# Kernel optimization log

Hardware: AMD Instinct MI355X
Metric: run time of the kernel (lower is better)

## Reference

```python
import jax, jax.numpy as jnp
import numpy as np

B, S, F, O = 128, 8, 32, 16  # batch, board_size, in_features, out_features
D = 2 * S - 1                # diff_size = 15 relative offsets per axis


def setup_inputs() -> dict:
    key = jax.random.key(0)
    k1, k2, k3 = jax.random.split(key, 3)
    inp = jax.random.normal(k1, (B, S, S, F), dtype=jnp.float32)
    # torch.nn.Bilinear init: U(-1/sqrt(in1_features), 1/sqrt(in1_features))
    bound = 1.0 / np.sqrt(F)
    W = jax.random.uniform(k2, (D, D, O, F, F), jnp.float32, -bound, bound)
    b = jax.random.uniform(k3, (D, D, O), jnp.float32, -bound, bound)
    return {"inp": inp, "W": W, "b": b}


def reference(inp, W, b):
    # inp: (B, S, S, F); W: (D, D, O, F, F); b: (D, D, O)
    s = inp.shape[1]
    idx = jnp.arange(s)
    # offset index: off[a, bb] = bb - a + (s - 1), in [0, 2s-2]
    off = idx[None, :] - idx[:, None] + (s - 1)  # (S, S)
    # gather per-pair bilinear weights: Wg[ax, bx, ay, by] = W[bx-ax+7, by-ay+7]
    Wg = W[off[:, :, None, None], off[None, None, :, :]]  # (S,S,S,S,O,F,F)
    bg = b[off[:, :, None, None], off[None, None, :, :]]  # (S,S,S,S,O) [ax,bx,ay,by]
    # out[b, ax, ay, bx, by, o] = a_i W_oij b_j + bias_o
    out = jnp.einsum('bxyi,xXyYoij,bXYj->bxyXYo', inp, Wg, inp)
    out = out + bg.transpose(0, 2, 1, 3, 4)[None]  # bias to [ax,ay,bx,by,o]
    return out
```

## Files before the change

kernel.cpp:

```cpp
#include <hip/hip_runtime.h>

typedef _Float16 f16;
typedef _Float16 f16x8 __attribute__((ext_vector_type(8)));
typedef float f32x4 __attribute__((ext_vector_type(4)));
typedef unsigned int u32;
typedef const __attribute__((address_space(1))) u32* gas1_t;
typedef __attribute__((address_space(3))) u32* las3_t;

#define WGRAN 460800
#define IGRAN 32768

__global__ __launch_bounds__(256) void convert_kernel(
    const float* __restrict__ W, const float* __restrict__ inp,
    f16* __restrict__ W_h, f16* __restrict__ inp_h)
{
    const int g = blockIdx.x * 256 + threadIdx.x;
    if (g < WGRAN) {
        const int dxdy = g >> 11;
        const int r = g & 2047;
        const int i = r >> 6, o = (r >> 2) & 15, quad = r & 3;
        const float* src = W + (size_t)dxdy * 16384 + o * 1024 + i * 32 + quad * 8;
        const float4 v0 = *(const float4*)src;
        const float4 v1 = *(const float4*)(src + 4);
        f16x8 h = { (f16)v0.x, (f16)v0.y, (f16)v0.z, (f16)v0.w,
                    (f16)v1.x, (f16)v1.y, (f16)v1.z, (f16)v1.w };
        *(f16x8*)(W_h + (size_t)g * 8) = h;
    } else {
        const int k = g - WGRAN;
        const float* src = inp + (size_t)k * 8;
        const float4 v0 = *(const float4*)src;
        const float4 v1 = *(const float4*)(src + 4);
        f16x8 h = { (f16)v0.x, (f16)v0.y, (f16)v0.z, (f16)v0.w,
                    (f16)v1.x, (f16)v1.y, (f16)v1.z, (f16)v1.w };
        *(f16x8*)(inp_h + (size_t)k * 8) = h;
    }
}

__global__ __launch_bounds__(256, 5) void rel_mfma3(
    const f16* __restrict__ W_h,
    const f16* __restrict__ inp_h,
    const float* __restrict__ bias,
    float* __restrict__ out)
{
    extern __shared__ __align__(16) f16 Wl[];

    const int hw = blockIdx.x;
    const int bid = ((hw & 7) << 9) | (hw >> 3);
    const int Y = bid & 7, X = (bid >> 3) & 7, y = (bid >> 6) & 7, x = (bid >> 9) & 7;
    const int dx = X - x + 7, dy = Y - y + 7;
    const int dxdy = dx * 15 + dy;

    const int t = threadIdx.x;

    {
        const f16* base = W_h + (size_t)dxdy * 16384;
        #pragma unroll
        for (int it = 0; it < 8; ++it) {
            const int idx = (it * 256 + t) * 8;
            __builtin_amdgcn_global_load_lds((gas1_t)(base + idx),
                                             (las3_t)&Wl[idx], 16, 0, 0);
        }
    }

    const int lane = t & 63;
    const int wave = t >> 6;
    const int quad = lane >> 4;
    const int m = lane & 15;

    f16x8 a0[4], a1[4], c0, c1;
    {
        const int b0 = wave * 32 + m;
        const int b1 = b0 + 16;
        const f16* ar0 = inp_h + ((b0 * 8 + x) * 8 + y) * 32;
        const f16* ar1 = inp_h + ((b1 * 8 + x) * 8 + y) * 32;
        #pragma unroll
        for (int g = 0; g < 4; ++g) {
            a0[g] = *(const f16x8*)(ar0 + g * 8);
            a1[g] = *(const f16x8*)(ar1 + g * 8);
        }
        c0 = *(const f16x8*)(inp_h + ((b0 * 8 + X) * 8 + Y) * 32 + quad * 8);
        c1 = *(const f16x8*)(inp_h + ((b1 * 8 + X) * 8 + Y) * 32 + quad * 8);
    }

    __syncthreads();

    f32x4 acc0 = {0.f, 0.f, 0.f, 0.f};
    f32x4 acc1 = {0.f, 0.f, 0.f, 0.f};
    const f16* wl = &Wl[m * 32 + quad * 8];
    f16x8 bfrag = *(const f16x8*)(wl);
    #pragma unroll
    for (int kb = 0; kb < 32; ++kb) {
        const f16x8 bcur = bfrag;
        if (kb < 31)
            bfrag = *(const f16x8*)(wl + (kb + 1) * 512);
        const f16 av0 = a0[kb >> 3][kb & 7];
        const f16 av1 = a1[kb >> 3][kb & 7];
        const f16x8 af0 = c0 * av0;
        const f16x8 af1 = c1 * av1;
        acc0 = __builtin_amdgcn_mfma_f32_16x16x32_f16(af0, bcur, acc0, 0, 0, 0);
        acc1 = __builtin_amdgcn_mfma_f32_16x16x32_f16(af1, bcur, acc1, 0, 0, 0);
    }

    const float bv = bias[dxdy * 16 + m];
    #pragma unroll
    for (int r = 0; r < 4; ++r) {
        const int b0 = wave * 32 + quad * 4 + r;
        out[((size_t)b0 * 4096 + bid) * 16 + m] = acc0[r] + bv;
        out[((size_t)(b0 + 16) * 4096 + bid) * 16 + m] = acc1[r] + bv;
    }
}

extern "C" void kernel_launch(void* const* d_in, const int* in_sizes, int n_in,
                              void* d_out, int out_size, void* d_ws, size_t ws_size,
                              hipStream_t stream)
{
    const float* inp  = (const float*)d_in[0];
    const float* W    = (const float*)d_in[1];
    const float* bias = (const float*)d_in[2];
    float* out = (float*)d_out;

    f16* W_h   = (f16*)d_ws;
    f16* inp_h = (f16*)d_ws + (size_t)WGRAN * 8;

    hipLaunchKernelGGL(convert_kernel, dim3((WGRAN + IGRAN) / 256), dim3(256), 0,
                       stream, W, inp, W_h, inp_h);
    hipLaunchKernelGGL(rel_mfma3, dim3(4096), dim3(256), 32768, stream,
                       W_h, inp_h, bias, out);
}
```

Before: 105.6 us.

## Loop over Y per block with double-buffered LDS weight prefetch

Each block now handles all 8 Y positions for a fixed (x,y,X), loading input rows once and iterating Y. The next Y's weight slice is prefetched into a second LDS buffer while the current one is consumed. This cuts the block count eightfold and doubles LDS use, reducing parallelism and occupancy in exchange for overlap and reuse.

```diff
diff --git a/kernel.cpp b/kernel.cpp
--- a/kernel.cpp
+++ b/kernel.cpp
@@ -36,7 +36,7 @@
     }
 }
 
-__global__ __launch_bounds__(256, 5) void rel_mfma3(
+__global__ __launch_bounds__(256, 2) void rel_mfma4(
     const f16* __restrict__ W_h,
     const f16* __restrict__ inp_h,
     const float* __restrict__ bias,
@@ -45,32 +45,28 @@
     extern __shared__ __align__(16) f16 Wl[];
 
     const int hw = blockIdx.x;
-    const int bid = ((hw & 7) << 9) | (hw >> 3);
-    const int Y = bid & 7, X = (bid >> 3) & 7, y = (bid >> 6) & 7, x = (bid >> 9) & 7;
-    const int dx = X - x + 7, dy = Y - y + 7;
-    const int dxdy = dx * 15 + dy;
+    const int X = hw & 7, y = (hw >> 3) & 7, x = (hw >> 6) & 7;
+    const int dx = X - x + 7;
 
     const int t = threadIdx.x;
-
-    {
-        const f16* base = W_h + (size_t)dxdy * 16384;
-        #pragma unroll
-        for (int it = 0; it < 8; ++it) {
-            const int idx = (it * 256 + t) * 8;
-            __builtin_amdgcn_global_load_lds((gas1_t)(base + idx),
-                                             (las3_t)&Wl[idx], 16, 0, 0);
-        }
-    }
-
     const int lane = t & 63;
     const int wave = t >> 6;
     const int quad = lane >> 4;
     const int m = lane & 15;
 
-    f16x8 a0[4], a1[4], c0, c1;
+    const f16* wbase = W_h + (size_t)(dx * 15 + 7 - y) * 16384;
+
+    #pragma unroll
+    for (int it = 0; it < 8; ++it) {
+        const int idx = (it * 256 + t) * 8;
+        __builtin_amdgcn_global_load_lds((gas1_t)(wbase + idx),
+                                         (las3_t)&Wl[idx], 16, 0, 0);
+    }
+
+    f16x8 a0[4], a1[4], c0[8], c1[8];
+    const int b0 = wave * 32 + m;
+    const int b1 = b0 + 16;
     {
-        const int b0 = wave * 32 + m;
-        const int b1 = b0 + 16;
         const f16* ar0 = inp_h + ((b0 * 8 + x) * 8 + y) * 32;
         const f16* ar1 = inp_h + ((b1 * 8 + x) * 8 + y) * 32;
         #pragma unroll
@@ -78,35 +74,62 @@
             a0[g] = *(const f16x8*)(ar0 + g * 8);
             a1[g] = *(const f16x8*)(ar1 + g * 8);
         }
-        c0 = *(const f16x8*)(inp_h + ((b0 * 8 + X) * 8 + Y) * 32 + quad * 8);
-        c1 = *(const f16x8*)(inp_h + ((b1 * 8 + X) * 8 + Y) * 32 + quad * 8);
+        const f16* cr0 = inp_h + (b0 * 8 + X) * 256 + quad * 8;
+        const f16* cr1 = inp_h + (b1 * 8 + X) * 256 + quad * 8;
+        #pragma unroll
+        for (int Yi = 0; Yi < 8; ++Yi) {
+            c0[Yi] = *(const f16x8*)(cr0 + Yi * 32);
+            c1[Yi] = *(const f16x8*)(cr1 + Yi * 32);
+        }
     }
 
     __syncthreads();
 
-    f32x4 acc0 = {0.f, 0.f, 0.f, 0.f};
-    f32x4 acc1 = {0.f, 0.f, 0.f, 0.f};
-    const f16* wl = &Wl[m * 32 + quad * 8];
-    f16x8 bfrag = *(const f16x8*)(wl);
+    const int bid_base = ((x * 8 + y) * 8 + X) * 8;
+
     #pragma unroll
-    for (int kb = 0; kb < 32; ++kb) {
-        const f16x8 bcur = bfrag;
-        if (kb < 31)
-            bfrag = *(const f16x8*)(wl + (kb + 1) * 512);
-        const f16 av0 = a0[kb >> 3][kb & 7];
-        const f16 av1 = a1[kb >> 3][kb & 7];
-        const f16x8 af0 = c0 * av0;
-        const f16x8 af1 = c1 * av1;
-        acc0 = __builtin_amdgcn_mfma_f32_16x16x32_f16(af0, bcur, acc0, 0, 0, 0);
-        acc1 = __builtin_amdgcn_mfma_f32_16x16x32_f16(af1, bcur, acc1, 0, 0, 0);
-    }
+    for (int Y = 0; Y < 8; ++Y) {
+        const int cur = Y & 1;
 
-    const float bv = bias[dxdy * 16 + m];
-    #pragma unroll
-    for (int r = 0; r < 4; ++r) {
-        const int b0 = wave * 32 + quad * 4 + r;
-        out[((size_t)b0 * 4096 + bid) * 16 + m] = acc0[r] + bv;
-        out[((size_t)(b0 + 16) * 4096 + bid) * 16 + m] = acc1[r] + bv;
+        if (Y < 7) {
+            const f16* nbase = wbase + (size_t)(Y + 1) * 16384;
+            f16* ldst = Wl + (cur ^ 1) * 16384;
+            #pragma unroll
+            for (int it = 0; it < 8; ++it) {
+                const int idx = (it * 256 + t) * 8;
+                __builtin_amdgcn_global_load_lds((gas1_t)(nbase + idx),
+                                                 (las3_t)&ldst[idx], 16, 0, 0);
+            }
+        }
+
+        f32x4 acc0 = {0.f, 0.f, 0.f, 0.f};
+        f32x4 acc1 = {0.f, 0.f, 0.f, 0.f};
+        const f16* wl = Wl + cur * 16384 + m * 32 + quad * 8;
+        f16x8 bfrag = *(const f16x8*)(wl);
+        #pragma unroll
+        for (int kb = 0; kb < 32; ++kb) {
+            const f16x8 bcur = bfrag;
+            if (kb < 31)
+                bfrag = *(const f16x8*)(wl + (kb + 1) * 512);
+            const f16 av0 = a0[kb >> 3][kb & 7];
+            const f16 av1 = a1[kb >> 3][kb & 7];
+            const f16x8 af0 = c0[Y] * av0;
+            const f16x8 af1 = c1[Y] * av1;
+            acc0 = __builtin_amdgcn_mfma_f32_16x16x32_f16(af0, bcur, acc0, 0, 0, 0);
+            acc1 = __builtin_amdgcn_mfma_f32_16x16x32_f16(af1, bcur, acc1, 0, 0, 0);
+        }
+
+        const int dxdy = dx * 15 + (Y - y + 7);
+        const int bid = bid_base + Y;
+        const float bv = bias[dxdy * 16 + m];
+        #pragma unroll
+        for (int r = 0; r < 4; ++r) {
+            const int bb = wave * 32 + quad * 4 + r;
+            out[((size_t)bb * 4096 + bid) * 16 + m]        = acc0[r] + bv;
+            out[((size_t)(bb + 16) * 4096 + bid) * 16 + m] = acc1[r] + bv;
+        }
+
+        __syncthreads();
     }
 }
 
@@ -124,6 +147,6 @@
 
     hipLaunchKernelGGL(convert_kernel, dim3((WGRAN + IGRAN) / 256), dim3(256), 0,
                        stream, W, inp, W_h, inp_h);
-    hipLaunchKernelGGL(rel_mfma3, dim3(4096), dim3(256), 32768, stream,
+    hipLaunchKernelGGL(rel_mfma4, dim3(512), dim3(256), 65536, stream,
                        W_h, inp_h, bias, out);
 }
```

Result: no change. 105.8 us (+0.2%).
